# Kernel tuning notes

Measured on AMD Instinct MI355X. Metric: run time of the kernel, lower is better.

Reference implementation:

```python
import jax, jax.numpy as jnp
import numpy as np

N_NODES = 50000
N_EDGES = 800000
N_GRAPHS = 128
IN_CH = 31
HID = 64
EPS = 1e-5


def _glorot(key, shape, scale=0.05):
    return jax.random.normal(key, shape, dtype=jnp.float32) * scale


def setup_inputs() -> dict:
    key = jax.random.key(0)
    ks = jax.random.split(key, 16)
    x = jax.random.normal(ks[0], (N_NODES, IN_CH), dtype=jnp.float32)
    edge_index = jax.random.randint(ks[1], (2, N_EDGES), 0, N_NODES, dtype=jnp.int32)
    batch = jnp.sort(jax.random.randint(ks[2], (N_NODES,), 0, N_GRAPHS, dtype=jnp.int32))
    params = {
        "t": jnp.ones((1,), dtype=jnp.float32),  # shared learnable softmax temperature
        "W1r": _glorot(ks[3], (HID, IN_CH)), "b1": jnp.zeros((HID,), jnp.float32), "W1s": _glorot(ks[4], (HID, IN_CH)),
        "W2r": _glorot(ks[5], (HID, HID)),  "b2": jnp.zeros((HID,), jnp.float32), "W2s": _glorot(ks[6], (HID, HID)),
        "W3r": _glorot(ks[7], (HID, HID)),  "b3": jnp.zeros((HID,), jnp.float32), "W3s": _glorot(ks[8], (HID, HID)),
        "Wl1": _glorot(ks[9], (2 * HID, 3 * HID)), "bl1": jnp.zeros((2 * HID,), jnp.float32),
        "Wl2": _glorot(ks[10], (HID // 2, 2 * HID)), "bl2": jnp.zeros((HID // 2,), jnp.float32),
    }
    return {"x": x, "edge_index": edge_index, "batch": batch, **params}


def _softmax_aggr(m, dst, t, n):
    # segment-softmax over incoming edges, per channel: alpha = softmax(t*m | dst)
    logits = m * t  # [E, C]
    mx = jax.ops.segment_max(logits, dst, num_segments=n)  # [N, C]
    e = jnp.exp(logits - mx[dst])
    denom = jax.ops.segment_sum(e, dst, num_segments=n)
    alpha = e / denom[dst]
    return jax.ops.segment_sum(m * alpha, dst, num_segments=n)  # [N, C]


def _graph_conv(x, src, dst, t, Wr, br, Ws):
    # PyG GraphConv: out = lin_rel(aggr_j x_j) + lin_root(x); lin_root has no bias
    m = x[src]  # gather [E, C]
    aggr = _softmax_aggr(m, dst, t, x.shape[0])
    return aggr @ Wr.T + br + x @ Ws.T


def _instance_norm(x):
    # torch InstanceNorm1d on [N, C] input -> normalize each row over feature dim
    mu = jnp.mean(x, axis=1, keepdims=True)
    var = jnp.mean((x - mu) ** 2, axis=1, keepdims=True)
    return (x - mu) / jnp.sqrt(var + EPS)


def reference(x, edge_index, batch, t, W1r, b1, W1s, W2r, b2, W2s, W3r, b3, W3s, Wl1, bl1, Wl2, bl2):
    src, dst = edge_index[0], edge_index[1]
    x1 = jax.nn.relu(_instance_norm(_graph_conv(x, src, dst, t, W1r, b1, W1s)))
    x2 = jax.nn.relu(_instance_norm(_graph_conv(x1, src, dst, t, W2r, b2, W2s)))
    x3 = jax.nn.relu(_instance_norm(_graph_conv(x2, src, dst, t, W3r, b3, W3s)))
    h1 = jax.ops.segment_max(x1, batch, num_segments=N_GRAPHS)
    h2 = jax.ops.segment_max(x2, batch, num_segments=N_GRAPHS)
    h3 = jax.ops.segment_max(x3, batch, num_segments=N_GRAPHS)
    h = jnp.concatenate([h1, h2, h3], axis=1)  # [G, 3*HID]
    z = jax.nn.relu(h @ Wl1.T + bl1)  # dropout is identity in eval mode
    z = z @ Wl2.T + bl2
    norm = jnp.maximum(jnp.linalg.norm(z, axis=1, keepdims=True), 1e-12)
    return z / norm
```

## Files before the change

### kernel.cpp

```cpp
#include <hip/hip_runtime.h>

#define N_NODES 50000
#define N_EDGES 800000
#define N_GRAPHS 128
#define IN_CH 31
#define HID 64

typedef __attribute__((ext_vector_type(8))) short short8;
typedef __attribute__((ext_vector_type(8))) unsigned short ushort8;
typedef __attribute__((ext_vector_type(4))) float floatx4;

__device__ inline unsigned f2bf(float f) {
    union { float f; unsigned u; } v; v.f = f;
    unsigned r = v.u + 0x7fff + ((v.u >> 16) & 1);
    return r >> 16;
}
__device__ inline float bf2f(unsigned short u) {
    union { unsigned u; float f; } v; v.u = ((unsigned)u) << 16; return v.f;
}
__device__ inline void pack4(short* p, float4 v) {
    unsigned lo = f2bf(v.x) | (f2bf(v.y) << 16);
    unsigned hi = f2bf(v.z) | (f2bf(v.w) << 16);
    *(uint2*)p = make_uint2(lo, hi);
}

__global__ void x2bf_kernel(const float* __restrict__ x, unsigned short* __restrict__ xb, int ntot) {
    int i = blockIdx.x * 256 + threadIdx.x;
    if (i < ntot) xb[i] = (unsigned short)f2bf(x[i]);
}


#define BKT_SHIFT 7
#define BKT_MAX 512
#define CHUNK 8192

__global__ void bucket_hist_kernel(const int* __restrict__ dst,
                                   int* __restrict__ bucket_cnt, int e, int nb) {
    __shared__ int bins[BKT_MAX];
    int tid = threadIdx.x;
    int i0 = blockIdx.x * CHUNK;
    int i1 = i0 + CHUNK; if (i1 > e) i1 = e;
    for (int k = tid; k < nb; k += 256) bins[k] = 0;
    __syncthreads();
    for (int j = i0 + tid; j < i1; j += 256)
        atomicAdd(&bins[dst[j] >> BKT_SHIFT], 1);
    __syncthreads();
    for (int k = tid; k < nb; k += 256)
        if (bins[k]) atomicAdd(&bucket_cnt[k], bins[k]);
}

__global__ void bucket_scan_kernel(const int* __restrict__ bucket_cnt,
                                   int* __restrict__ bucket_off,
                                   int* __restrict__ bucket_cur,
                                   int* __restrict__ row_ptr, int nb, int nN, int e) {
    __shared__ int s[512];
    int tid = threadIdx.x;
    int v = (tid < nb) ? bucket_cnt[tid] : 0;
    s[tid] = v;
    __syncthreads();
    for (int off = 1; off < 512; off <<= 1) {
        int u = (tid >= off) ? s[tid - off] : 0;
        __syncthreads();
        s[tid] += u;
        __syncthreads();
    }
    if (tid < nb) {
        int excl = s[tid] - v;
        bucket_off[tid] = excl;
        bucket_cur[tid] = excl;
    }
    if (tid == 0) {
        bucket_off[nb] = e;
        row_ptr[nN] = e;
    }
}

__global__ void bucket_scatter_kernel(const int* __restrict__ src,
                                      const int* __restrict__ dst,
                                      int* __restrict__ bucket_cur,
                                      int2* __restrict__ ebuf, int e, int nb) {
    __shared__ int bins[BKT_MAX];
    __shared__ int base[BKT_MAX];
    __shared__ int lcur[BKT_MAX];
    int tid = threadIdx.x;
    int i0 = blockIdx.x * CHUNK;
    int i1 = i0 + CHUNK; if (i1 > e) i1 = e;
    for (int k = tid; k < nb; k += 256) { bins[k] = 0; lcur[k] = 0; }
    __syncthreads();
    for (int j = i0 + tid; j < i1; j += 256)
        atomicAdd(&bins[dst[j] >> BKT_SHIFT], 1);
    __syncthreads();
    for (int k = tid; k < nb; k += 256)
        if (bins[k]) base[k] = atomicAdd(&bucket_cur[k], bins[k]);
    __syncthreads();
    for (int j = i0 + tid; j < i1; j += 256) {
        int ss = src[j], dd = dst[j];
        int b = dd >> BKT_SHIFT;
        int p = atomicAdd(&lcur[b], 1);
        ebuf[base[b] + p] = make_int2(ss, dd);
    }
}

__global__ void bucket_csr_kernel(const int2* __restrict__ ebuf,
                                  const int* __restrict__ bucket_off,
                                  int* __restrict__ row_ptr,
                                  int* __restrict__ csr_src, int nN) {
    __shared__ int nh[128];
    __shared__ int s[128];
    __shared__ int ncur[128];
    int tid = threadIdx.x;
    int b = blockIdx.x;
    int boff = bucket_off[b], bend = bucket_off[b + 1];
    int node0 = b << BKT_SHIFT;
    if (tid < 128) nh[tid] = 0;
    __syncthreads();
    for (int j = boff + tid; j < bend; j += 256)
        atomicAdd(&nh[ebuf[j].y - node0], 1);
    __syncthreads();
    int v = (tid < 128) ? nh[tid] : 0;
    if (tid < 128) s[tid] = v;
    __syncthreads();
    for (int off = 1; off < 128; off <<= 1) {
        int u = (tid < 128 && tid >= off) ? s[tid - off] : 0;
        __syncthreads();
        if (tid < 128) s[tid] += u;
        __syncthreads();
    }
    if (tid < 128 && node0 + tid < nN) {
        int excl = boff + s[tid] - v;
        row_ptr[node0 + tid] = excl;
        ncur[tid] = excl;
    }
    __syncthreads();
    for (int j = boff + tid; j < bend; j += 256) {
        int2 ed = ebuf[j];
        int pos = atomicAdd(&ncur[ed.y - node0], 1);
        csr_src[pos] = ed.x;
    }
}


__global__ void gstart_kernel(const int* __restrict__ batch, int* __restrict__ gstart, int nN) {
    int i = blockIdx.x * 256 + threadIdx.x;
    if (i >= nN) return;
    int b = batch[i];
    int bp = (i == 0) ? -1 : batch[i - 1];
    for (int g = bp + 1; g <= b; ++g) gstart[g] = i;
    if (i == nN - 1)
        for (int g = b + 1; g <= N_GRAPHS; ++g) gstart[g] = nN;
}

__global__ void __launch_bounds__(1024) gmax_kernel(const unsigned short* __restrict__ y,
                                                    const int* __restrict__ gstart,
                                                    float* __restrict__ hout) {
    __shared__ float sm[16][64];
    int g = blockIdx.x;
    int tid = threadIdx.x, w = tid >> 6, l = tid & 63;
    int s0 = gstart[g], s1 = gstart[g + 1];
    float m = 0.f;
    for (int i = s0 + w; i < s1; i += 16)
        m = fmaxf(m, bf2f(y[(size_t)i * 64 + l]));
    sm[w][l] = m;
    __syncthreads();
    if (w == 0) {
        #pragma unroll
        for (int k = 1; k < 16; ++k) m = fmaxf(m, sm[k][l]);
        hout[g * 64 + l] = m;
    }
}


template <int C_IN>
__global__ void __launch_bounds__(256, 8) aggr_kernel(
        const unsigned short* __restrict__ xin, const float* __restrict__ tptr,
        const int* __restrict__ row_ptr, const int* __restrict__ csr_src,
        unsigned short* __restrict__ aRowsB, int n) {
    int w = threadIdx.x >> 6, l = threadIdx.x & 63;
    int d = blockIdx.x * 4 + w;
    if (d >= n) return;
    float tval = tptr[0];
    int beg = __builtin_amdgcn_readfirstlane(row_ptr[d]);
    int end = __builtin_amdgcn_readfirstlane(row_ptr[d + 1]);
    int half = l >> 5;

    if constexpr (C_IN == 64) {
        int co = (l & 31) * 2;
        float2 num2 = {0.f, 0.f}, den2 = {0.f, 0.f};
        int base = beg;
        for (; base + 64 <= end; base += 64) {
            int sidx = csr_src[base + l];
            #pragma unroll
            for (int j = 0; j < 64; j += 16) {
                float2 v[8];
                #pragma unroll
                for (int p = 0; p < 8; ++p) {
                    int sa = __builtin_amdgcn_readlane(sidx, j + 2 * p);
                    int sb = __builtin_amdgcn_readlane(sidx, j + 2 * p + 1);
                    int s  = half ? sb : sa;
                    ushort2 u = *(const ushort2*)&xin[(size_t)s * 64 + co];
                    v[p].x = bf2f(u.x); v[p].y = bf2f(u.y);
                }
                #pragma unroll
                for (int p = 0; p < 8; ++p) {
                    float ex = __expf(tval * v[p].x);
                    float ey = __expf(tval * v[p].y);
                    den2.x += ex; den2.y += ey;
                    num2.x = fmaf(v[p].x, ex, num2.x);
                    num2.y = fmaf(v[p].y, ey, num2.y);
                }
            }
        }
        int rem = end - base;
        if (rem > 0) {
            int sidx = csr_src[base + ((l < rem) ? l : 0)];
            for (int j = 0; j < rem; j += 16) {
                float2 v[8];
                #pragma unroll
                for (int p = 0; p < 8; ++p) {
                    int ja = j + 2 * p;     if (ja >= rem) ja = rem - 1;
                    int jb = j + 2 * p + 1; if (jb >= rem) jb = rem - 1;
                    int sa = __builtin_amdgcn_readlane(sidx, ja);
                    int sb = __builtin_amdgcn_readlane(sidx, jb);
                    int s  = half ? sb : sa;
                    ushort2 u = *(const ushort2*)&xin[(size_t)s * 64 + co];
                    v[p].x = bf2f(u.x); v[p].y = bf2f(u.y);
                }
                #pragma unroll
                for (int p = 0; p < 8; ++p) {
                    float m = (j + 2 * p + half < rem) ? 1.f : 0.f;
                    float ex = __expf(tval * v[p].x) * m;
                    float ey = __expf(tval * v[p].y) * m;
                    den2.x += ex; den2.y += ey;
                    num2.x = fmaf(v[p].x, ex, num2.x);
                    num2.y = fmaf(v[p].y, ey, num2.y);
                }
            }
        }
        num2.x += __shfl_xor(num2.x, 32);
        num2.y += __shfl_xor(num2.y, 32);
        den2.x += __shfl_xor(den2.x, 32);
        den2.y += __shfl_xor(den2.y, 32);
        float nx = __shfl(num2.x, l >> 1);
        float ny = __shfl(num2.y, l >> 1);
        float dx = __shfl(den2.x, l >> 1);
        float dy = __shfl(den2.y, l >> 1);
        float num = (l & 1) ? ny : nx;
        float den = (l & 1) ? dy : dx;
        float aggr = (end > beg) ? num / den : 0.f;
        aRowsB[(size_t)d * 64 + l] = (unsigned short)f2bf(aggr);
    } else {
        int ch = l & 31;
        int chc = (ch < C_IN) ? ch : (C_IN - 1);
        float num = 0.f, den = 0.f;
        int base = beg;
        for (; base + 64 <= end; base += 64) {
            int sidx = csr_src[base + l];
            #pragma unroll
            for (int j = 0; j < 64; j += 16) {
                float v[8];
                #pragma unroll
                for (int p = 0; p < 8; ++p) {
                    int sa = __builtin_amdgcn_readlane(sidx, j + 2 * p);
                    int sb = __builtin_amdgcn_readlane(sidx, j + 2 * p + 1);
                    int s  = half ? sb : sa;
                    v[p] = bf2f(xin[(size_t)s * C_IN + chc]);
                }
                #pragma unroll
                for (int p = 0; p < 8; ++p) {
                    float e = __expf(tval * v[p]);
                    den += e;
                    num = fmaf(v[p], e, num);
                }
            }
        }
        int rem = end - base;
        if (rem > 0) {
            int sidx = csr_src[base + ((l < rem) ? l : 0)];
            for (int j = 0; j < rem; j += 16) {
                float v[8];
                #pragma unroll
                for (int p = 0; p < 8; ++p) {
                    int ja = j + 2 * p;     if (ja >= rem) ja = rem - 1;
                    int jb = j + 2 * p + 1; if (jb >= rem) jb = rem - 1;
                    int sa = __builtin_amdgcn_readlane(sidx, ja);
                    int sb = __builtin_amdgcn_readlane(sidx, jb);
                    int s  = half ? sb : sa;
                    v[p] = bf2f(xin[(size_t)s * C_IN + chc]);
                }
                #pragma unroll
                for (int p = 0; p < 8; ++p) {
                    float m = (j + 2 * p + half < rem) ? 1.f : 0.f;
                    float e = __expf(tval * v[p]) * m;
                    den += e;
                    num = fmaf(v[p], e, num);
                }
            }
        }
        num += __shfl_xor(num, 32);
        den += __shfl_xor(den, 32);
        float aggr = (end > beg && den > 0.f) ? num / den : 0.f;
        unsigned short outv;
        if (l < C_IN)               outv = (unsigned short)f2bf(aggr);
        else if (l < 2 * C_IN)      outv = xin[(size_t)d * C_IN + (l - C_IN)];
        else                        outv = 0;
        aRowsB[(size_t)d * 64 + l] = outv;
    }
}


template <int C_IN>
__global__ void __launch_bounds__(256, 4) transform_kernel(
        const unsigned short* __restrict__ aRowsB, const unsigned short* __restrict__ yprev,
        const float* __restrict__ Wr, const float* __restrict__ br,
        const float* __restrict__ Ws,
        unsigned short* __restrict__ yout, int n) {
    constexpr int K_TOT = (C_IN == 64) ? 128 : 64;
    constexpr int KP    = K_TOT + 8;
    constexpr int KS    = K_TOT / 32;
    constexpr int ABSH  = 2 * 64 * KP;
    constexpr int CSH   = 64 * 68 * 2;
    constexpr int SMSH  = (ABSH > CSH) ? ABSH : CSH;

    __shared__ short smem[SMSH];
    short* sA = smem;
    short* sB = smem + 64 * KP;
    float* sC = (float*)smem;

    int tid = threadIdx.x;
    int nb = blockIdx.x * 64;

    if constexpr (C_IN == 64) {
        for (int idx = tid; idx < 64 * 16; idx += 256) {
            int row = idx >> 4, c8 = idx & 15;
            int node = nb + row; if (node >= n) node = n - 1;
            ushort8 v = (c8 < 8) ? ((const ushort8*)(aRowsB + (size_t)node * 64))[c8]
                                 : ((const ushort8*)(yprev + (size_t)node * 64))[c8 - 8];
            *(ushort8*)&sA[row * KP + c8 * 8] = v;
        }
        for (int idx = tid; idx < 64 * 32; idx += 256) {
            int nr = idx >> 5, c4 = idx & 31;
            float4 v = (c4 < 16) ? ((const float4*)(Wr + nr * 64))[c4]
                                 : ((const float4*)(Ws + nr * 64))[c4 - 16];
            pack4(&sB[nr * KP + c4 * 4], v);
        }
    } else {
        for (int idx = tid; idx < 64 * 8; idx += 256) {
            int row = idx >> 3, c8 = idx & 7;
            int node = nb + row; if (node >= n) node = n - 1;
            ushort8 v = ((const ushort8*)(aRowsB + (size_t)node * 64))[c8];
            *(ushort8*)&sA[row * KP + c8 * 8] = v;
        }
        for (int idx = tid; idx < 64 * 64; idx += 256) {
            int nr = idx >> 6, k = idx & 63;
            float v = (k < C_IN) ? Wr[nr * C_IN + k]
                    : (k < 2 * C_IN) ? Ws[nr * C_IN + (k - C_IN)] : 0.f;
            sB[nr * KP + k] = (short)f2bf(v);
        }
    }
    __syncthreads();

    int w = tid >> 6, l = tid & 63;
    int m = l & 15;
    int q = l >> 4;
    floatx4 acc[4] = {{0.f,0.f,0.f,0.f},{0.f,0.f,0.f,0.f},
                      {0.f,0.f,0.f,0.f},{0.f,0.f,0.f,0.f}};
    const short* aBase = &sA[(w * 16 + m) * KP + q * 8];
    #pragma unroll 2
    for (int s = 0; s < KS; ++s) {
        short8 af = *(const short8*)(aBase + s * 32);
        #pragma unroll
        for (int t = 0; t < 4; ++t) {
            short8 bf = *(const short8*)&sB[(t * 16 + m) * KP + q * 8 + s * 32];
            acc[t] = __builtin_amdgcn_mfma_f32_16x16x32_bf16(af, bf, acc[t], 0, 0, 0);
        }
    }

    __syncthreads();
    #pragma unroll
    for (int t = 0; t < 4; ++t)
        #pragma unroll
        for (int r = 0; r < 4; ++r)
            sC[(w * 16 + q * 4 + r) * 68 + t * 16 + m] = acc[t][r];
    __syncthreads();

    float bias = br[l];
    for (int i = 0; i < 16; ++i) {
        int j = w * 16 + i;
        int d = nb + j;
        if (d < n) {
            float a = sC[j * 68 + l] + bias;
            float s = a;
            for (int off = 32; off > 0; off >>= 1) s += __shfl_xor(s, off);
            float mu = s * (1.0f / 64.0f);
            float dc = a - mu;
            float s2 = dc * dc;
            for (int off = 32; off > 0; off >>= 1) s2 += __shfl_xor(s2, off);
            float var = s2 * (1.0f / 64.0f);
            float y = dc * rsqrtf(var + 1e-5f);
            y = fmaxf(y, 0.f);
            yout[(size_t)d * 64 + l] = (unsigned short)f2bf(y);
        }
    }
}


__global__ void mlp_kernel(const float* __restrict__ h,
                           const float* __restrict__ Wl1, const float* __restrict__ bl1,
                           const float* __restrict__ Wl2, const float* __restrict__ bl2,
                           float* __restrict__ out) {
    __shared__ float hrow[192];
    __shared__ float z1[128];
    __shared__ float z2[32];
    __shared__ float snorm;
    int g = blockIdx.x, tid = threadIdx.x;
    if (tid < 64) {
        hrow[tid]       = h[0 * N_GRAPHS * 64 + g * 64 + tid];
        hrow[64 + tid]  = h[1 * N_GRAPHS * 64 + g * 64 + tid];
        hrow[128 + tid] = h[2 * N_GRAPHS * 64 + g * 64 + tid];
    }
    __syncthreads();
    float acc = bl1[tid];
    #pragma unroll 8
    for (int c = 0; c < 192; ++c) acc = fmaf(hrow[c], Wl1[tid * 192 + c], acc);
    z1[tid] = fmaxf(acc, 0.f);
    __syncthreads();
    if (tid < 32) {
        float a2 = bl2[tid];
        #pragma unroll 8
        for (int c = 0; c < 128; ++c) a2 = fmaf(z1[c], Wl2[tid * 128 + c], a2);
        z2[tid] = a2;
    }
    __syncthreads();
    if (tid == 0) {
        float ss = 0.f;
        for (int i = 0; i < 32; ++i) ss += z2[i] * z2[i];
        snorm = fmaxf(sqrtf(ss), 1e-12f);
    }
    __syncthreads();
    if (tid < 32) out[g * 32 + tid] = z2[tid] / snorm;
}


extern "C" void kernel_launch(void* const* d_in, const int* in_sizes, int n_in,
                              void* d_out, int out_size, void* d_ws, size_t ws_size,
                              hipStream_t stream) {
    const float* x   = (const float*)d_in[0];
    const int* eidx  = (const int*)d_in[1];
    const int* batch = (const int*)d_in[2];
    const float* t   = (const float*)d_in[3];
    const float* W1r = (const float*)d_in[4];
    const float* b1  = (const float*)d_in[5];
    const float* W1s = (const float*)d_in[6];
    const float* W2r = (const float*)d_in[7];
    const float* b2  = (const float*)d_in[8];
    const float* W2s = (const float*)d_in[9];
    const float* W3r = (const float*)d_in[10];
    const float* b3  = (const float*)d_in[11];
    const float* W3s = (const float*)d_in[12];
    const float* Wl1 = (const float*)d_in[13];
    const float* bl1 = (const float*)d_in[14];
    const float* Wl2 = (const float*)d_in[15];
    const float* bl2 = (const float*)d_in[16];
    float* out = (float*)d_out;

    const int nE = in_sizes[1] / 2;
    const int nN = in_sizes[2];
    const int* src = eidx;
    const int* dst = eidx + nE;
    const int nb = (nN + 127) >> BKT_SHIFT;

    char* ws = (char*)d_ws;
    size_t off = 0;
    auto alloc = [&](size_t bytes) {
        char* p = ws + off;
        off = (off + bytes + 255) & ~(size_t)255;
        return p;
    };
    int*            bucket_cnt = (int*)alloc((size_t)(nb + 1) * 4);
    int*            bucket_off = (int*)alloc((size_t)(nb + 1) * 4);
    int*            bucket_cur = (int*)alloc((size_t)(nb + 1) * 4);
    int*            gstart     = (int*)alloc((size_t)(N_GRAPHS + 1) * 4);
    float*          h          = (float*)alloc((size_t)3 * N_GRAPHS * 64 * 4);
    int*            row_ptr    = (int*)alloc((size_t)(nN + 1) * 4);
    int2*           ebuf       = (int2*)alloc((size_t)nE * 8);
    int*            csr_src    = (int*)alloc((size_t)nE * 4);
    unsigned short* xbf        = (unsigned short*)alloc((size_t)nN * IN_CH * 2);
    unsigned short* aRowsB     = (unsigned short*)alloc((size_t)nN * 64 * 2);
    unsigned short* yAb        = (unsigned short*)alloc((size_t)nN * 64 * 2);
    unsigned short* yBb        = (unsigned short*)alloc((size_t)nN * 64 * 2);

    const int nbChunk = (nE + CHUNK - 1) / CHUNK;
    const int nbN     = (nN + 255) / 256;

    hipMemsetAsync(bucket_cnt, 0, (size_t)(nb + 1) * 4, stream);
    x2bf_kernel<<<(nN * IN_CH + 255) / 256, 256, 0, stream>>>(x, xbf, nN * IN_CH);
    bucket_hist_kernel<<<nbChunk, 256, 0, stream>>>(dst, bucket_cnt, nE, nb);
    bucket_scan_kernel<<<1, 512, 0, stream>>>(bucket_cnt, bucket_off, bucket_cur,
                                              row_ptr, nb, nN, nE);
    bucket_scatter_kernel<<<nbChunk, 256, 0, stream>>>(src, dst, bucket_cur, ebuf, nE, nb);
    bucket_csr_kernel<<<nb, 256, 0, stream>>>(ebuf, bucket_off, row_ptr, csr_src, nN);
    gstart_kernel<<<nbN, 256, 0, stream>>>(batch, gstart, nN);

    const int nbA = (nN + 3) / 4;
    const int nbT = (nN + 63) / 64;

    aggr_kernel<IN_CH><<<nbA, 256, 0, stream>>>(xbf, t, row_ptr, csr_src, aRowsB, nN);
    transform_kernel<IN_CH><<<nbT, 256, 0, stream>>>(aRowsB, nullptr,
                                                     W1r, b1, W1s, yAb, nN);
    gmax_kernel<<<N_GRAPHS, 1024, 0, stream>>>(yAb, gstart, h + 0 * N_GRAPHS * 64);

    aggr_kernel<HID><<<nbA, 256, 0, stream>>>(yAb, t, row_ptr, csr_src, aRowsB, nN);
    transform_kernel<HID><<<nbT, 256, 0, stream>>>(aRowsB, yAb,
                                                   W2r, b2, W2s, yBb, nN);
    gmax_kernel<<<N_GRAPHS, 1024, 0, stream>>>(yBb, gstart, h + 1 * N_GRAPHS * 64);

    aggr_kernel<HID><<<nbA, 256, 0, stream>>>(yBb, t, row_ptr, csr_src, aRowsB, nN);
    transform_kernel<HID><<<nbT, 256, 0, stream>>>(aRowsB, yBb,
                                                   W3r, b3, W3s, yAb, nN);
    gmax_kernel<<<N_GRAPHS, 1024, 0, stream>>>(yAb, gstart, h + 2 * N_GRAPHS * 64);

    mlp_kernel<<<N_GRAPHS, 128, 0, stream>>>(h, Wl1, bl1, Wl2, bl2, out);
}
```

Before: 315.6 us.

## Precompute per-node softmax exp and weighted value as packed fp16 pairs

Moves the exp(t*x) and x*exp(t*x) computation from per-edge in the aggregation kernels to per-node in the producer (prep and transform kernels), storing them as packed half2. The aggregation then only gathers and sums these pairs. This removes one exp per edge-channel in exchange for doubling the gathered bytes per edge and using fp16 precision, which risks overflow or accuracy loss. It also omits the max-subtraction, as before.

```diff
diff --git a/kernel.cpp b/kernel.cpp
--- a/kernel.cpp
+++ b/kernel.cpp
@@ -1,4 +1,5 @@
 #include <hip/hip_runtime.h>
+#include <hip/hip_fp16.h>
 
 #define N_NODES 50000
 #define N_EDGES 800000
@@ -23,10 +24,30 @@
     unsigned hi = f2bf(v.z) | (f2bf(v.w) << 16);
     *(uint2*)p = make_uint2(lo, hi);
 }
-
-__global__ void x2bf_kernel(const float* __restrict__ x, unsigned short* __restrict__ xb, int ntot) {
+__device__ inline unsigned packEP(float E, float P) {
+    __half2 h = __floats2half2_rn(E, P);
+    return *(unsigned*)&h;
+}
+__device__ inline float2 unpackEP(unsigned u) {
+    __half2 h = *(__half2*)&u;
+    return __half22float2(h);
+}
+
+__global__ void prep_kernel(const float* __restrict__ x, const float* __restrict__ tptr,
+                            unsigned short* __restrict__ xbf, unsigned* __restrict__ EP0,
+                            int nN) {
     int i = blockIdx.x * 256 + threadIdx.x;
-    if (i < ntot) xb[i] = (unsigned short)f2bf(x[i]);
+    if (i >= nN * 32) return;
+    int node = i >> 5, c = i & 31;
+    if (c < IN_CH) {
+        float xv = x[node * IN_CH + c];
+        xbf[node * IN_CH + c] = (unsigned short)f2bf(xv);
+        float tval = tptr[0];
+        float E = __expf(tval * xv);
+        EP0[i] = packEP(E, xv * E);
+    } else {
+        EP0[i] = 0;
+    }
 }
 
 
@@ -172,41 +193,38 @@
 
 template <int C_IN>
 __global__ void __launch_bounds__(256, 8) aggr_kernel(
-        const unsigned short* __restrict__ xin, const float* __restrict__ tptr,
+        const unsigned* __restrict__ EP, const unsigned short* __restrict__ xin,
         const int* __restrict__ row_ptr, const int* __restrict__ csr_src,
         unsigned short* __restrict__ aRowsB, int n) {
     int w = threadIdx.x >> 6, l = threadIdx.x & 63;
     int d = blockIdx.x * 4 + w;
     if (d >= n) return;
-    float tval = tptr[0];
     int beg = __builtin_amdgcn_readfirstlane(row_ptr[d]);
     int end = __builtin_amdgcn_readfirstlane(row_ptr[d + 1]);
     int half = l >> 5;
 
     if constexpr (C_IN == 64) {
-        int co = (l & 31) * 2;
+        int co = l & 31;
         float2 num2 = {0.f, 0.f}, den2 = {0.f, 0.f};
         int base = beg;
         for (; base + 64 <= end; base += 64) {
             int sidx = csr_src[base + l];
             #pragma unroll
             for (int j = 0; j < 64; j += 16) {
-                float2 v[8];
+                uint2 v[8];
                 #pragma unroll
                 for (int p = 0; p < 8; ++p) {
                     int sa = __builtin_amdgcn_readlane(sidx, j + 2 * p);
                     int sb = __builtin_amdgcn_readlane(sidx, j + 2 * p + 1);
                     int s  = half ? sb : sa;
-                    ushort2 u = *(const ushort2*)&xin[(size_t)s * 64 + co];
-                    v[p].x = bf2f(u.x); v[p].y = bf2f(u.y);
-                }
-                #pragma unroll
-                for (int p = 0; p < 8; ++p) {
-                    float ex = __expf(tval * v[p].x);
-                    float ey = __expf(tval * v[p].y);
-                    den2.x += ex; den2.y += ey;
-                    num2.x = fmaf(v[p].x, ex, num2.x);
-                    num2.y = fmaf(v[p].y, ey, num2.y);
+                    v[p] = *(const uint2*)&EP[(size_t)s * 64 + 2 * co];
+                }
+                #pragma unroll
+                for (int p = 0; p < 8; ++p) {
+                    float2 e0 = unpackEP(v[p].x);
+                    float2 e1 = unpackEP(v[p].y);
+                    den2.x += e0.x; num2.x += e0.y;
+                    den2.y += e1.x; num2.y += e1.y;
                 }
             }
         }
@@ -214,7 +232,7 @@
         if (rem > 0) {
             int sidx = csr_src[base + ((l < rem) ? l : 0)];
             for (int j = 0; j < rem; j += 16) {
-                float2 v[8];
+                uint2 v[8];
                 #pragma unroll
                 for (int p = 0; p < 8; ++p) {
                     int ja = j + 2 * p;     if (ja >= rem) ja = rem - 1;
@@ -222,17 +240,15 @@
                     int sa = __builtin_amdgcn_readlane(sidx, ja);
                     int sb = __builtin_amdgcn_readlane(sidx, jb);
                     int s  = half ? sb : sa;
-                    ushort2 u = *(const ushort2*)&xin[(size_t)s * 64 + co];
-                    v[p].x = bf2f(u.x); v[p].y = bf2f(u.y);
+                    v[p] = *(const uint2*)&EP[(size_t)s * 64 + 2 * co];
                 }
                 #pragma unroll
                 for (int p = 0; p < 8; ++p) {
                     float m = (j + 2 * p + half < rem) ? 1.f : 0.f;
-                    float ex = __expf(tval * v[p].x) * m;
-                    float ey = __expf(tval * v[p].y) * m;
-                    den2.x += ex; den2.y += ey;
-                    num2.x = fmaf(v[p].x, ex, num2.x);
-                    num2.y = fmaf(v[p].y, ey, num2.y);
+                    float2 e0 = unpackEP(v[p].x);
+                    float2 e1 = unpackEP(v[p].y);
+                    den2.x = fmaf(e0.x, m, den2.x); num2.x = fmaf(e0.y, m, num2.x);
+                    den2.y = fmaf(e1.x, m, den2.y); num2.y = fmaf(e1.y, m, num2.y);
                 }
             }
         }
@@ -246,7 +262,7 @@
         float dy = __shfl(den2.y, l >> 1);
         float num = (l & 1) ? ny : nx;
         float den = (l & 1) ? dy : dx;
-        float aggr = (end > beg) ? num / den : 0.f;
+        float aggr = (end > beg && den > 0.f) ? num / den : 0.f;
         aRowsB[(size_t)d * 64 + l] = (unsigned short)f2bf(aggr);
     } else {
         int ch = l & 31;
@@ -257,19 +273,19 @@
             int sidx = csr_src[base + l];
             #pragma unroll
             for (int j = 0; j < 64; j += 16) {
-                float v[8];
+                unsigned v[8];
                 #pragma unroll
                 for (int p = 0; p < 8; ++p) {
                     int sa = __builtin_amdgcn_readlane(sidx, j + 2 * p);
                     int sb = __builtin_amdgcn_readlane(sidx, j + 2 * p + 1);
                     int s  = half ? sb : sa;
-                    v[p] = bf2f(xin[(size_t)s * C_IN + chc]);
-                }
-                #pragma unroll
-                for (int p = 0; p < 8; ++p) {
-                    float e = __expf(tval * v[p]);
-                    den += e;
-                    num = fmaf(v[p], e, num);
+                    v[p] = EP[(size_t)s * 32 + chc];
+                }
+                #pragma unroll
+                for (int p = 0; p < 8; ++p) {
+                    float2 e = unpackEP(v[p]);
+                    den += e.x;
+                    num += e.y;
                 }
             }
         }
@@ -277,7 +293,7 @@
         if (rem > 0) {
             int sidx = csr_src[base + ((l < rem) ? l : 0)];
             for (int j = 0; j < rem; j += 16) {
-                float v[8];
+                unsigned v[8];
                 #pragma unroll
                 for (int p = 0; p < 8; ++p) {
                     int ja = j + 2 * p;     if (ja >= rem) ja = rem - 1;
@@ -285,14 +301,14 @@
                     int sa = __builtin_amdgcn_readlane(sidx, ja);
                     int sb = __builtin_amdgcn_readlane(sidx, jb);
                     int s  = half ? sb : sa;
-                    v[p] = bf2f(xin[(size_t)s * C_IN + chc]);
+                    v[p] = EP[(size_t)s * 32 + chc];
                 }
                 #pragma unroll
                 for (int p = 0; p < 8; ++p) {
                     float m = (j + 2 * p + half < rem) ? 1.f : 0.f;
-                    float e = __expf(tval * v[p]) * m;
-                    den += e;
-                    num = fmaf(v[p], e, num);
+                    float2 e = unpackEP(v[p]);
+                    den = fmaf(e.x, m, den);
+                    num = fmaf(e.y, m, num);
                 }
             }
         }
@@ -308,12 +324,12 @@
 }
 
 
-template <int C_IN>
+template <int C_IN, bool WEP>
 __global__ void __launch_bounds__(256, 4) transform_kernel(
         const unsigned short* __restrict__ aRowsB, const unsigned short* __restrict__ yprev,
         const float* __restrict__ Wr, const float* __restrict__ br,
-        const float* __restrict__ Ws,
-        unsigned short* __restrict__ yout, int n) {
+        const float* __restrict__ Ws, const float* __restrict__ tptr,
+        unsigned short* __restrict__ yout, unsigned* __restrict__ EPout, int n) {
     constexpr int K_TOT = (C_IN == 64) ? 128 : 64;
     constexpr int KP    = K_TOT + 8;
     constexpr int KS    = K_TOT / 32;
@@ -384,6 +400,8 @@
     __syncthreads();
 
     float bias = br[l];
+    float tval = 0.f;
+    if constexpr (WEP) tval = tptr[0];
     for (int i = 0; i < 16; ++i) {
         int j = w * 16 + i;
         int d = nb + j;
@@ -399,6 +417,10 @@
             float y = dc * rsqrtf(var + 1e-5f);
             y = fmaxf(y, 0.f);
             yout[(size_t)d * 64 + l] = (unsigned short)f2bf(y);
+            if constexpr (WEP) {
+                float E = __expf(tval * y);
+                EPout[(size_t)d * 64 + l] = packEP(E, y * E);
+            }
         }
     }
 }
@@ -485,6 +507,8 @@
     int2*           ebuf       = (int2*)alloc((size_t)nE * 8);
     int*            csr_src    = (int*)alloc((size_t)nE * 4);
     unsigned short* xbf        = (unsigned short*)alloc((size_t)nN * IN_CH * 2);
+    unsigned*       EP0        = (unsigned*)alloc((size_t)nN * 32 * 4);
+    unsigned*       EPbuf      = (unsigned*)alloc((size_t)nN * 64 * 4);
     unsigned short* aRowsB     = (unsigned short*)alloc((size_t)nN * 64 * 2);
     unsigned short* yAb        = (unsigned short*)alloc((size_t)nN * 64 * 2);
     unsigned short* yBb        = (unsigned short*)alloc((size_t)nN * 64 * 2);
@@ -493,7 +517,7 @@
     const int nbN     = (nN + 255) / 256;
 
     hipMemsetAsync(bucket_cnt, 0, (size_t)(nb + 1) * 4, stream);
-    x2bf_kernel<<<(nN * IN_CH + 255) / 256, 256, 0, stream>>>(x, xbf, nN * IN_CH);
+    prep_kernel<<<(nN * 32 + 255) / 256, 256, 0, stream>>>(x, t, xbf, EP0, nN);
     bucket_hist_kernel<<<nbChunk, 256, 0, stream>>>(dst, bucket_cnt, nE, nb);
     bucket_scan_kernel<<<1, 512, 0, stream>>>(bucket_cnt, bucket_off, bucket_cur,
                                               row_ptr, nb, nN, nE);
@@ -504,19 +528,19 @@
     const int nbA = (nN + 3) / 4;
     const int nbT = (nN + 63) / 64;
 
-    aggr_kernel<IN_CH><<<nbA, 256, 0, stream>>>(xbf, t, row_ptr, csr_src, aRowsB, nN);
-    transform_kernel<IN_CH><<<nbT, 256, 0, stream>>>(aRowsB, nullptr,
-                                                     W1r, b1, W1s, yAb, nN);
+    aggr_kernel<IN_CH><<<nbA, 256, 0, stream>>>(EP0, xbf, row_ptr, csr_src, aRowsB, nN);
+    transform_kernel<IN_CH, true><<<nbT, 256, 0, stream>>>(aRowsB, nullptr,
+                                                           W1r, b1, W1s, t, yAb, EPbuf, nN);
     gmax_kernel<<<N_GRAPHS, 1024, 0, stream>>>(yAb, gstart, h + 0 * N_GRAPHS * 64);
 
-    aggr_kernel<HID><<<nbA, 256, 0, stream>>>(yAb, t, row_ptr, csr_src, aRowsB, nN);
-    transform_kernel<HID><<<nbT, 256, 0, stream>>>(aRowsB, yAb,
-                                                   W2r, b2, W2s, yBb, nN);
+    aggr_kernel<HID><<<nbA, 256, 0, stream>>>(EPbuf, nullptr, row_ptr, csr_src, aRowsB, nN);
+    transform_kernel<HID, true><<<nbT, 256, 0, stream>>>(aRowsB, yAb,
+                                                         W2r, b2, W2s, t, yBb, EPbuf, nN);
     gmax_kernel<<<N_GRAPHS, 1024, 0, stream>>>(yBb, gstart, h + 1 * N_GRAPHS * 64);
 
-    aggr_kernel<HID><<<nbA, 256, 0, stream>>>(yBb, t, row_ptr, csr_src, aRowsB, nN);
-    transform_kernel<HID><<<nbT, 256, 0, stream>>>(aRowsB, yBb,
-                                                   W3r, b3, W3s, yAb, nN);
+    aggr_kernel<HID><<<nbA, 256, 0, stream>>>(EPbuf, nullptr, row_ptr, csr_src, aRowsB, nN);
+    transform_kernel<HID, false><<<nbT, 256, 0, stream>>>(aRowsB, yBb,
+                                                          W3r, b3, W3s, t, yAb, nullptr, nN);
     gmax_kernel<<<N_GRAPHS, 1024, 0, stream>>>(yAb, gstart, h + 2 * N_GRAPHS * 64);
 
     mlp_kernel<<<N_GRAPHS, 128, 0, stream>>>(h, Wl1, bl1, Wl2, bl2, out);
```

Result: no change. 309.8 us (-1.8%).
